# Performance work log

Hardware: AMD Instinct MI355X
Metric: run time of the kernel (lower is better)

## Reference

```python
import jax, jax.numpy as jnp
import numpy as np

N_NODES = 50000
N_EDGES = 800000


def _gcn_layer(x, edges, W, b):
    # support = x @ W  (dense transform first: cheaper when out_dim < in_dim)
    support = x @ W  # [N, D_out]
    src, dst = edges[0], edges[1]
    # sparse neighbor aggregation: sum_{(s,d) in E} support[s] into node d
    agg = jax.ops.segment_sum(support[src], dst, num_segments=x.shape[0])
    return agg + b


def setup_inputs() -> dict:
    key = jax.random.key(0)
    k1, k2, k3, k4, k5, k6 = jax.random.split(key, 6)
    x = jax.random.normal(k1, (N_NODES, 512), dtype=jnp.float32)
    edges = jax.random.randint(k2, (2, N_EDGES), 0, N_NODES, dtype=jnp.int32)
    W1 = jax.random.normal(k3, (512, 256), dtype=jnp.float32) * 0.05
    b1 = jax.random.normal(k4, (256,), dtype=jnp.float32) * 0.05
    W2 = jax.random.normal(k5, (256, 128), dtype=jnp.float32) * 0.05
    b2 = jax.random.normal(k6, (128,), dtype=jnp.float32) * 0.05
    return {"x": x, "edges": edges, "W1": W1, "b1": b1, "W2": W2, "b2": b2}


def reference(x, edges, W1, b1, W2, b2):
    x1 = jax.nn.relu(_gcn_layer(x, edges, W1, b1))
    x2 = jax.nn.relu(_gcn_layer(x1, edges, W2, b2))
    return x2
```

## Files before the change

### kernel.cpp

```cpp
#include <hip/hip_runtime.h>

#define N_NODES 50000
#define N_EDGES 800000
#define MP 50176
#define CAP 64

typedef unsigned short ushort_t;
typedef unsigned int uint_t;
using short8 = __attribute__((ext_vector_type(8))) short;
using f32x4 = __attribute__((ext_vector_type(4))) float;
using floatx2 = __attribute__((ext_vector_type(2))) float;
using int4v = __attribute__((ext_vector_type(4))) int;
using uint4v = __attribute__((ext_vector_type(4))) uint_t;

__device__ __forceinline__ ushort_t f2bf(float f) {
    uint_t u;
    __builtin_memcpy(&u, &f, 4);
    u = u + 0x7FFF + ((u >> 16) & 1);
    return (ushort_t)(u >> 16);
}

__global__ __launch_bounds__(256) void prep(const float* __restrict__ W1,
                                            const float* __restrict__ W2,
                                            ushort_t* __restrict__ W1t,
                                            ushort_t* __restrict__ W2t,
                                            int* __restrict__ cnt) {
    const int i = blockIdx.x * blockDim.x + threadIdx.x;
    if (i < 256 * 512) {
        const int n = i >> 9, k = i & 511;
        W1t[i] = f2bf(W1[(size_t)k * 256 + n]);
    }
    if (i < 128 * 256) {
        const int n = i >> 8, k = i & 255;
        W2t[i] = f2bf(W2[(size_t)k * 128 + n]);
    }
    if (i < N_NODES) cnt[i] = 0;
}

__global__ __launch_bounds__(256) void csr_fill_bucket(
    const int* __restrict__ eg, int* __restrict__ cnt,
    int* __restrict__ csrp) {
    constexpr int PART = N_NODES / 8;
    const int part = blockIdx.x & 7;
    const int q = blockIdx.x >> 3;
    const int lo = part * PART;
    const int hi = lo + PART;
    const int stride = (gridDim.x >> 3) * 256;
    for (int e = q * 256 + threadIdx.x; e < N_EDGES; e += stride) {
        const int d = eg[N_EDGES + e];
        if (d >= lo && d < hi) {
            const int slot = atomicAdd(&cnt[d], 1);
            if (slot < CAP) csrp[(size_t)d * CAP + slot] = eg[e];
        }
    }
}

template <int K, int BN, bool AF32, bool CFP8>
__global__ __launch_bounds__(512) void gemm_mfma(const void* __restrict__ Av,
                                                 const ushort_t* __restrict__ Bt,
                                                 void* __restrict__ Cv) {
    constexpr int KT = K / 64;
    constexpr int NF = BN / 64;
    constexpr int BSL = (BN == 256) ? 4 : 2;
    __shared__ ushort_t lA[128 * 64];
    __shared__ ushort_t lB[BN * 64];
    const int tid = threadIdx.x;
    const int w = tid >> 6, lane = tid & 63;
    const int wr = w >> 2, wc = w & 3;
    const int m0 = blockIdx.x * 128;

    const int ar = tid >> 2, aq0 = (tid & 3) * 2;
    const int br = (BN == 256) ? (tid >> 1) : (tid >> 2);
    const int bs0 = (BN == 256) ? ((tid & 1) * 4) : ((tid & 3) * 2);

    int agr = m0 + ar;
    if (AF32 && agr >= N_NODES) agr = 0;

    f32x4 acc[4][NF];
#pragma unroll
    for (int m = 0; m < 4; ++m)
#pragma unroll
        for (int n = 0; n < NF; ++n) acc[m][n] = (f32x4){0.f, 0.f, 0.f, 0.f};

    float4 fa[4];
    int4v ha0, ha1;
    int4v rB[BSL];

    auto LOAD = [&](int kt) {
        if constexpr (AF32) {
            const float* Af = (const float*)Av;
            const float4* p =
                (const float4*)(Af + (size_t)agr * K + kt * 64 + aq0 * 8);
#pragma unroll
            for (int i = 0; i < 4; ++i) fa[i] = p[i];
        } else {
            const ushort_t* Ab = (const ushort_t*)Av;
            const int4v* p =
                (const int4v*)(Ab + (size_t)(m0 + ar) * K + kt * 64 + aq0 * 8);
            ha0 = p[0];
            ha1 = p[1];
        }
        const int4v* qp = (const int4v*)(Bt + (size_t)br * K + kt * 64 + bs0 * 8);
#pragma unroll
        for (int s = 0; s < BSL; ++s) rB[s] = qp[s];
    };

    auto STORE = [&]() {
        short8 oa0, oa1;
        if constexpr (AF32) {
            oa0[0] = (short)f2bf(fa[0].x); oa0[1] = (short)f2bf(fa[0].y);
            oa0[2] = (short)f2bf(fa[0].z); oa0[3] = (short)f2bf(fa[0].w);
            oa0[4] = (short)f2bf(fa[1].x); oa0[5] = (short)f2bf(fa[1].y);
            oa0[6] = (short)f2bf(fa[1].z); oa0[7] = (short)f2bf(fa[1].w);
            oa1[0] = (short)f2bf(fa[2].x); oa1[1] = (short)f2bf(fa[2].y);
            oa1[2] = (short)f2bf(fa[2].z); oa1[3] = (short)f2bf(fa[2].w);
            oa1[4] = (short)f2bf(fa[3].x); oa1[5] = (short)f2bf(fa[3].y);
            oa1[6] = (short)f2bf(fa[3].z); oa1[7] = (short)f2bf(fa[3].w);
        } else {
            __builtin_memcpy(&oa0, &ha0, 16);
            __builtin_memcpy(&oa1, &ha1, 16);
        }
        *(short8*)((char*)lA + ar * 128 + ((aq0 ^ (ar & 7)) << 4)) = oa0;
        *(short8*)((char*)lA + ar * 128 + (((aq0 + 1) ^ (ar & 7)) << 4)) = oa1;
#pragma unroll
        for (int s = 0; s < BSL; ++s) {
            short8 ob;
            __builtin_memcpy(&ob, &rB[s], 16);
            *(short8*)((char*)lB + br * 128 + (((bs0 + s) ^ (br & 7)) << 4)) = ob;
        }
    };

    LOAD(0);
    STORE();
    __syncthreads();

    for (int kt = 0; kt < KT; ++kt) {
        if (kt + 1 < KT) LOAD(kt + 1);
        __builtin_amdgcn_sched_barrier(0);
        const int g = lane >> 4, rr = lane & 15;
#pragma unroll
        for (int kk = 0; kk < 2; ++kk) {
            short8 av[4], bv[NF];
#pragma unroll
            for (int m = 0; m < 4; ++m) {
                const int row = wr * 64 + m * 16 + rr;
                av[m] = *(const short8*)((const char*)lA + row * 128 +
                                         (((kk * 4 + g) ^ (row & 7)) << 4));
            }
#pragma unroll
            for (int n = 0; n < NF; ++n) {
                const int row = wc * (BN / 4) + n * 16 + rr;
                bv[n] = *(const short8*)((const char*)lB + row * 128 +
                                         (((kk * 4 + g) ^ (row & 7)) << 4));
            }
#pragma unroll
            for (int m = 0; m < 4; ++m)
#pragma unroll
                for (int n = 0; n < NF; ++n)
                    acc[m][n] = __builtin_amdgcn_mfma_f32_16x16x32_bf16(
                        av[m], bv[n], acc[m][n], 0, 0, 0);
        }
        __syncthreads();
        if (kt + 1 < KT) {
            STORE();
            __syncthreads();
        }
    }

    const int rr = lane & 15, rg = lane >> 4;
#pragma unroll
    for (int m = 0; m < 4; ++m)
#pragma unroll
        for (int n = 0; n < NF; ++n) {
            const int row0 = m0 + wr * 64 + m * 16 + rg * 4;
            const int col = wc * (BN / 4) + n * 16 + rr;
            if constexpr (CFP8) {
                unsigned char* Cb = (unsigned char*)Cv;
                const int w01 = __builtin_amdgcn_cvt_pk_fp8_f32(
                    acc[m][n][0], acc[m][n][1], 0, false);
                const int w23 = __builtin_amdgcn_cvt_pk_fp8_f32(
                    acc[m][n][2], acc[m][n][3], 0, false);
                Cb[(size_t)(row0 + 0) * BN + col] = (unsigned char)(w01 & 0xff);
                Cb[(size_t)(row0 + 1) * BN + col] = (unsigned char)((w01 >> 8) & 0xff);
                Cb[(size_t)(row0 + 2) * BN + col] = (unsigned char)(w23 & 0xff);
                Cb[(size_t)(row0 + 3) * BN + col] = (unsigned char)((w23 >> 8) & 0xff);
            } else {
                ushort_t* Cs = (ushort_t*)Cv;
#pragma unroll
                for (int q = 0; q < 4; ++q)
                    Cs[(size_t)(row0 + q) * BN + col] = f2bf(acc[m][n][q]);
            }
        }
}

template <int D, bool MASKED>
__device__ __forceinline__ void chunk8_fp8(const unsigned char* __restrict__ S,
                                           const int* __restrict__ csr,
                                           int j, int end, int coff,
                                           float* __restrict__ acc) {
    int id[8];
#pragma unroll
    for (int q = 0; q < 8; ++q) {
        const int raw = csr[j + q];
        id[q] = (!MASKED || (j + q < end)) ? raw : 0;
    }
    uint4v v[8];
#pragma unroll
    for (int q = 0; q < 8; ++q)
        v[q] = *(const uint4v*)(S + (size_t)id[q] * D + coff);
#pragma unroll
    for (int q = 0; q < 8; ++q) {
        const float mq = MASKED ? ((j + q < end) ? 1.f : 0.f) : 1.f;
#pragma unroll
        for (int wd = 0; wd < 4; ++wd) {
            const int word = (int)v[q][wd];
            const floatx2 lo = __builtin_amdgcn_cvt_pk_f32_fp8(word, false);
            const floatx2 hi = __builtin_amdgcn_cvt_pk_f32_fp8(word, true);
            if (MASKED) {
                acc[wd * 4 + 0] = fmaf(mq, lo[0], acc[wd * 4 + 0]);
                acc[wd * 4 + 1] = fmaf(mq, lo[1], acc[wd * 4 + 1]);
                acc[wd * 4 + 2] = fmaf(mq, hi[0], acc[wd * 4 + 2]);
                acc[wd * 4 + 3] = fmaf(mq, hi[1], acc[wd * 4 + 3]);
            } else {
                acc[wd * 4 + 0] += lo[0];
                acc[wd * 4 + 1] += lo[1];
                acc[wd * 4 + 2] += hi[0];
                acc[wd * 4 + 3] += hi[1];
            }
        }
    }
}

template <int D, bool OUT_BF16>
__global__ __launch_bounds__(256) void gather_fp8(
    const unsigned char* __restrict__ S, const int* __restrict__ cnt,
    const int* __restrict__ csrp, const float* __restrict__ bias,
    void* __restrict__ out) {
    constexpr int LPN = D / 16;
    const int gtid = blockIdx.x * blockDim.x + threadIdx.x;
    const int node = gtid / LPN;
    const int l = gtid % LPN;
    if (node >= N_NODES) return;
    const int beg = node * CAP;
    const int deg = min(cnt[node], CAP);
    const int end = beg + deg;
    const int coff = l * 16;

    float acc[16];
#pragma unroll
    for (int k = 0; k < 16; ++k) acc[k] = 0.f;

    int j = beg;
    const int e8 = beg + (deg & ~7);
    for (; j < e8; j += 8) chunk8_fp8<D, false>(S, csrp, j, end, coff, acc);
    if (j < end) chunk8_fp8<D, true>(S, csrp, j, end, coff, acc);

#pragma unroll
    for (int k = 0; k < 16; ++k) acc[k] = fmaxf(acc[k] + bias[coff + k], 0.f);

    if (OUT_BF16) {
        short8 o0, o1;
#pragma unroll
        for (int k = 0; k < 8; ++k) {
            o0[k] = (short)f2bf(acc[k]);
            o1[k] = (short)f2bf(acc[8 + k]);
        }
        ushort_t* op = (ushort_t*)out + (size_t)node * D + coff;
        *(short8*)(op) = o0;
        *(short8*)(op + 8) = o1;
    } else {
        float* op = (float*)out + (size_t)node * D + coff;
        *(float4*)(op + 0)  = make_float4(acc[0], acc[1], acc[2], acc[3]);
        *(float4*)(op + 4)  = make_float4(acc[4], acc[5], acc[6], acc[7]);
        *(float4*)(op + 8)  = make_float4(acc[8], acc[9], acc[10], acc[11]);
        *(float4*)(op + 12) = make_float4(acc[12], acc[13], acc[14], acc[15]);
    }
}

extern "C" void kernel_launch(void* const* d_in, const int* in_sizes, int n_in,
                              void* d_out, int out_size, void* d_ws, size_t ws_size,
                              hipStream_t stream) {
    const float* x  = (const float*)d_in[0];
    const int*   eg = (const int*)d_in[1];
    const float* W1 = (const float*)d_in[2];
    const float* b1 = (const float*)d_in[3];
    const float* W2 = (const float*)d_in[4];
    const float* b2 = (const float*)d_in[5];
    float* out = (float*)d_out;

    char* ws = (char*)d_ws;
    const size_t SUP1_OFF = 0;
    const size_t AGG1_OFF = 25690112;
    const size_t SUP2_OFF = 51380224;
    const size_t W1T_OFF  = 77070336;
    const size_t W2T_OFF  = 77332480;
    const size_t CNT_OFF  = 77398016;
    const size_t CSRP_OFF = 77598208;

    unsigned char* sup1 = (unsigned char*)(ws + SUP1_OFF);
    ushort_t* agg1 = (ushort_t*)(ws + AGG1_OFF);
    unsigned char* sup2 = (unsigned char*)(ws + SUP2_OFF);
    ushort_t* W1t  = (ushort_t*)(ws + W1T_OFF);
    ushort_t* W2t  = (ushort_t*)(ws + W2T_OFF);
    int* cnt  = (int*)(ws + CNT_OFF);
    int* csrp = (int*)(ws + CSRP_OFF);

    prep<<<512, 256, 0, stream>>>(W1, W2, W1t, W2t, cnt);
    csr_fill_bucket<<<2048, 256, 0, stream>>>(eg, cnt, csrp);

    gemm_mfma<512, 256, true, true><<<MP / 128, 512, 0, stream>>>(x, W1t, sup1);
    gather_fp8<256, true><<<(N_NODES * 16 + 255) / 256, 256, 0, stream>>>(
        sup1, cnt, csrp, b1, agg1);

    gemm_mfma<256, 128, false, true><<<MP / 128, 512, 0, stream>>>(agg1, W2t, sup2);
    gather_fp8<128, false><<<(N_NODES * 8 + 255) / 256, 256, 0, stream>>>(
        sup2, cnt, csrp, b2, out);
}
```

Measured before the change: 142.4 us.

## Use direct global-to-LDS async loads with double-buffered tiles in both GEMMs

Splits the templated GEMM into two specialized kernels. B tiles (and A tiles in the second GEMM) are loaded straight into LDS with global_load_lds into double buffers, with pre-swizzled source addresses, so the register staging and LDS store pass go away and the next tile's load overlaps the current compute. The cost is more LDS per block (64KB+ for gemm1), which may lower occupancy. Correctness also depends on the async LDS writes being complete at the barriers, since no explicit vmcnt wait is added.

```diff
diff --git a/kernel.cpp b/kernel.cpp
--- a/kernel.cpp
+++ b/kernel.cpp
@@ -18,6 +18,12 @@
     __builtin_memcpy(&u, &f, 4);
     u = u + 0x7FFF + ((u >> 16) & 1);
     return (ushort_t)(u >> 16);
+}
+
+__device__ __forceinline__ void async_copy16(const void* g, void* l) {
+    __builtin_amdgcn_global_load_lds(
+        (const __attribute__((address_space(1))) uint_t*)g,
+        (__attribute__((address_space(3))) uint_t*)l, 16, 0, 0);
 }
 
 __global__ __launch_bounds__(256) void prep(const float* __restrict__ W1,
@@ -55,92 +61,75 @@
     }
 }
 
-template <int K, int BN, bool AF32, bool CFP8>
-__global__ __launch_bounds__(512) void gemm_mfma(const void* __restrict__ Av,
-                                                 const ushort_t* __restrict__ Bt,
-                                                 void* __restrict__ Cv) {
-    constexpr int KT = K / 64;
-    constexpr int NF = BN / 64;
-    constexpr int BSL = (BN == 256) ? 4 : 2;
+__global__ __launch_bounds__(512) void gemm1_k(const float* __restrict__ A,
+                                               const ushort_t* __restrict__ Bt,
+                                               unsigned char* __restrict__ C) {
+    constexpr int K = 512, BN = 256, KT = 8;
     __shared__ ushort_t lA[128 * 64];
-    __shared__ ushort_t lB[BN * 64];
+    __shared__ ushort_t lB[2][256 * 64];
     const int tid = threadIdx.x;
     const int w = tid >> 6, lane = tid & 63;
     const int wr = w >> 2, wc = w & 3;
     const int m0 = blockIdx.x * 128;
 
     const int ar = tid >> 2, aq0 = (tid & 3) * 2;
-    const int br = (BN == 256) ? (tid >> 1) : (tid >> 2);
-    const int bs0 = (BN == 256) ? ((tid & 1) * 4) : ((tid & 3) * 2);
+    const int sr = lane >> 3, sj = lane & 7;
 
     int agr = m0 + ar;
-    if (AF32 && agr >= N_NODES) agr = 0;
-
-    f32x4 acc[4][NF];
+    if (agr >= N_NODES) agr = 0;
+
+    f32x4 acc[4][4];
 #pragma unroll
     for (int m = 0; m < 4; ++m)
 #pragma unroll
-        for (int n = 0; n < NF; ++n) acc[m][n] = (f32x4){0.f, 0.f, 0.f, 0.f};
+        for (int n = 0; n < 4; ++n) acc[m][n] = (f32x4){0.f, 0.f, 0.f, 0.f};
 
     float4 fa[4];
-    int4v ha0, ha1;
-    int4v rB[BSL];
-
-    auto LOAD = [&](int kt) {
-        if constexpr (AF32) {
-            const float* Af = (const float*)Av;
-            const float4* p =
-                (const float4*)(Af + (size_t)agr * K + kt * 64 + aq0 * 8);
-#pragma unroll
-            for (int i = 0; i < 4; ++i) fa[i] = p[i];
-        } else {
-            const ushort_t* Ab = (const ushort_t*)Av;
-            const int4v* p =
-                (const int4v*)(Ab + (size_t)(m0 + ar) * K + kt * 64 + aq0 * 8);
-            ha0 = p[0];
-            ha1 = p[1];
-        }
-        const int4v* qp = (const int4v*)(Bt + (size_t)br * K + kt * 64 + bs0 * 8);
-#pragma unroll
-        for (int s = 0; s < BSL; ++s) rB[s] = qp[s];
+
+    auto LOAD_A = [&](int kt) {
+        const float4* p = (const float4*)(A + (size_t)agr * K + kt * 64 + aq0 * 8);
+#pragma unroll
+        for (int i = 0; i < 4; ++i) fa[i] = p[i];
     };
-
-    auto STORE = [&]() {
+    auto ISSUE_B = [&](int kt, int buf) {
+#pragma unroll
+        for (int i = 0; i < 4; ++i) {
+            const int r = w * 32 + i * 8 + sr;
+            const char* g = (const char*)Bt + ((size_t)r * K + kt * 64) * 2 +
+                            ((size_t)(sj ^ (r & 7)) << 4);
+            async_copy16(g, lB[buf] + (size_t)(w * 32 + i * 8) * 64);
+        }
+    };
+    auto STORE_A = [&]() {
         short8 oa0, oa1;
-        if constexpr (AF32) {
-            oa0[0] = (short)f2bf(fa[0].x); oa0[1] = (short)f2bf(fa[0].y);
-            oa0[2] = (short)f2bf(fa[0].z); oa0[3] = (short)f2bf(fa[0].w);
-            oa0[4] = (short)f2bf(fa[1].x); oa0[5] = (short)f2bf(fa[1].y);
-            oa0[6] = (short)f2bf(fa[1].z); oa0[7] = (short)f2bf(fa[1].w);
-            oa1[0] = (short)f2bf(fa[2].x); oa1[1] = (short)f2bf(fa[2].y);
-            oa1[2] = (short)f2bf(fa[2].z); oa1[3] = (short)f2bf(fa[2].w);
-            oa1[4] = (short)f2bf(fa[3].x); oa1[5] = (short)f2bf(fa[3].y);
-            oa1[6] = (short)f2bf(fa[3].z); oa1[7] = (short)f2bf(fa[3].w);
-        } else {
-            __builtin_memcpy(&oa0, &ha0, 16);
-            __builtin_memcpy(&oa1, &ha1, 16);
-        }
+        oa0[0] = (short)f2bf(fa[0].x); oa0[1] = (short)f2bf(fa[0].y);
+        oa0[2] = (short)f2bf(fa[0].z); oa0[3] = (short)f2bf(fa[0].w);
+        oa0[4] = (short)f2bf(fa[1].x); oa0[5] = (short)f2bf(fa[1].y);
+        oa0[6] = (short)f2bf(fa[1].z); oa0[7] = (short)f2bf(fa[1].w);
+        oa1[0] = (short)f2bf(fa[2].x); oa1[1] = (short)f2bf(fa[2].y);
+        oa1[2] = (short)f2bf(fa[2].z); oa1[3] = (short)f2bf(fa[2].w);
+        oa1[4] = (short)f2bf(fa[3].x); oa1[5] = (short)f2bf(fa[3].y);
+        oa1[6] = (short)f2bf(fa[3].z); oa1[7] = (short)f2bf(fa[3].w);
         *(short8*)((char*)lA + ar * 128 + ((aq0 ^ (ar & 7)) << 4)) = oa0;
         *(short8*)((char*)lA + ar * 128 + (((aq0 + 1) ^ (ar & 7)) << 4)) = oa1;
-#pragma unroll
-        for (int s = 0; s < BSL; ++s) {
-            short8 ob;
-            __builtin_memcpy(&ob, &rB[s], 16);
-            *(short8*)((char*)lB + br * 128 + (((bs0 + s) ^ (br & 7)) << 4)) = ob;
-        }
     };
 
-    LOAD(0);
-    STORE();
+    LOAD_A(0);
+    ISSUE_B(0, 0);
+    STORE_A();
     __syncthreads();
 
+    int cur = 0;
     for (int kt = 0; kt < KT; ++kt) {
-        if (kt + 1 < KT) LOAD(kt + 1);
+        if (kt + 1 < KT) {
+            ISSUE_B(kt + 1, cur ^ 1);
+            LOAD_A(kt + 1);
+        }
         __builtin_amdgcn_sched_barrier(0);
         const int g = lane >> 4, rr = lane & 15;
 #pragma unroll
         for (int kk = 0; kk < 2; ++kk) {
-            short8 av[4], bv[NF];
+            short8 av[4], bv[4];
 #pragma unroll
             for (int m = 0; m < 4; ++m) {
                 const int row = wr * 64 + m * 16 + rr;
@@ -148,21 +137,22 @@
                                          (((kk * 4 + g) ^ (row & 7)) << 4));
             }
 #pragma unroll
-            for (int n = 0; n < NF; ++n) {
-                const int row = wc * (BN / 4) + n * 16 + rr;
-                bv[n] = *(const short8*)((const char*)lB + row * 128 +
+            for (int n = 0; n < 4; ++n) {
+                const int row = wc * 64 + n * 16 + rr;
+                bv[n] = *(const short8*)((const char*)lB[cur] + row * 128 +
                                          (((kk * 4 + g) ^ (row & 7)) << 4));
             }
 #pragma unroll
             for (int m = 0; m < 4; ++m)
 #pragma unroll
-                for (int n = 0; n < NF; ++n)
+                for (int n = 0; n < 4; ++n)
                     acc[m][n] = __builtin_amdgcn_mfma_f32_16x16x32_bf16(
                         av[m], bv[n], acc[m][n], 0, 0, 0);
         }
         __syncthreads();
         if (kt + 1 < KT) {
-            STORE();
+            STORE_A();
+            cur ^= 1;
             __syncthreads();
         }
     }
@@ -171,25 +161,100 @@
 #pragma unroll
     for (int m = 0; m < 4; ++m)
 #pragma unroll
-        for (int n = 0; n < NF; ++n) {
+        for (int n = 0; n < 4; ++n) {
             const int row0 = m0 + wr * 64 + m * 16 + rg * 4;
-            const int col = wc * (BN / 4) + n * 16 + rr;
-            if constexpr (CFP8) {
-                unsigned char* Cb = (unsigned char*)Cv;
-                const int w01 = __builtin_amdgcn_cvt_pk_fp8_f32(
-                    acc[m][n][0], acc[m][n][1], 0, false);
-                const int w23 = __builtin_amdgcn_cvt_pk_fp8_f32(
-                    acc[m][n][2], acc[m][n][3], 0, false);
-                Cb[(size_t)(row0 + 0) * BN + col] = (unsigned char)(w01 & 0xff);
-                Cb[(size_t)(row0 + 1) * BN + col] = (unsigned char)((w01 >> 8) & 0xff);
-                Cb[(size_t)(row0 + 2) * BN + col] = (unsigned char)(w23 & 0xff);
-                Cb[(size_t)(row0 + 3) * BN + col] = (unsigned char)((w23 >> 8) & 0xff);
-            } else {
-                ushort_t* Cs = (ushort_t*)Cv;
-#pragma unroll
-                for (int q = 0; q < 4; ++q)
-                    Cs[(size_t)(row0 + q) * BN + col] = f2bf(acc[m][n][q]);
-            }
+            const int col = wc * 64 + n * 16 + rr;
+            const int w01 = __builtin_amdgcn_cvt_pk_fp8_f32(
+                acc[m][n][0], acc[m][n][1], 0, false);
+            const int w23 = __builtin_amdgcn_cvt_pk_fp8_f32(
+                acc[m][n][2], acc[m][n][3], 0, false);
+            C[(size_t)(row0 + 0) * BN + col] = (unsigned char)(w01 & 0xff);
+            C[(size_t)(row0 + 1) * BN + col] = (unsigned char)((w01 >> 8) & 0xff);
+            C[(size_t)(row0 + 2) * BN + col] = (unsigned char)(w23 & 0xff);
+            C[(size_t)(row0 + 3) * BN + col] = (unsigned char)((w23 >> 8) & 0xff);
+        }
+}
+
+__global__ __launch_bounds__(512) void gemm2_k(const ushort_t* __restrict__ A,
+                                               const ushort_t* __restrict__ Bt,
+                                               unsigned char* __restrict__ C) {
+    constexpr int K = 256, BN = 128, KT = 4;
+    __shared__ ushort_t lA[2][128 * 64];
+    __shared__ ushort_t lB[2][128 * 64];
+    const int tid = threadIdx.x;
+    const int w = tid >> 6, lane = tid & 63;
+    const int wr = w >> 2, wc = w & 3;
+    const int m0 = blockIdx.x * 128;
+    const int sr = lane >> 3, sj = lane & 7;
+
+    f32x4 acc[4][2];
+#pragma unroll
+    for (int m = 0; m < 4; ++m)
+#pragma unroll
+        for (int n = 0; n < 2; ++n) acc[m][n] = (f32x4){0.f, 0.f, 0.f, 0.f};
+
+    auto ISSUE = [&](int kt, int buf) {
+#pragma unroll
+        for (int i = 0; i < 2; ++i) {
+            const int r = w * 16 + i * 8 + sr;
+            const char* ga = (const char*)A + ((size_t)(m0 + r) * K + kt * 64) * 2 +
+                             ((size_t)(sj ^ (r & 7)) << 4);
+            async_copy16(ga, lA[buf] + (size_t)(w * 16 + i * 8) * 64);
+            const char* gb = (const char*)Bt + ((size_t)r * K + kt * 64) * 2 +
+                             ((size_t)(sj ^ (r & 7)) << 4);
+            async_copy16(gb, lB[buf] + (size_t)(w * 16 + i * 8) * 64);
+        }
+    };
+
+    ISSUE(0, 0);
+    __syncthreads();
+
+    int cur = 0;
+    for (int kt = 0; kt < KT; ++kt) {
+        if (kt + 1 < KT) ISSUE(kt + 1, cur ^ 1);
+        __builtin_amdgcn_sched_barrier(0);
+        const int g = lane >> 4, rr = lane & 15;
+#pragma unroll
+        for (int kk = 0; kk < 2; ++kk) {
+            short8 av[4], bv[2];
+#pragma unroll
+            for (int m = 0; m < 4; ++m) {
+                const int row = wr * 64 + m * 16 + rr;
+                av[m] = *(const short8*)((const char*)lA[cur] + row * 128 +
+                                         (((kk * 4 + g) ^ (row & 7)) << 4));
+            }
+#pragma unroll
+            for (int n = 0; n < 2; ++n) {
+                const int row = wc * 32 + n * 16 + rr;
+                bv[n] = *(const short8*)((const char*)lB[cur] + row * 128 +
+                                         (((kk * 4 + g) ^ (row & 7)) << 4));
+            }
+#pragma unroll
+            for (int m = 0; m < 4; ++m)
+#pragma unroll
+                for (int n = 0; n < 2; ++n)
+                    acc[m][n] = __builtin_amdgcn_mfma_f32_16x16x32_bf16(
+                        av[m], bv[n], acc[m][n], 0, 0, 0);
+        }
+        __syncthreads();
+        cur ^= 1;
+    }
+
+    const int rr = lane & 15, rg = lane >> 4;
+#pragma unroll
+    for (int m = 0; m < 4; ++m)
+#pragma unroll
+        for (int n = 0; n < 2; ++n) {
+            const int row0 = m0 + wr * 64 + m * 16 + rg * 4;
+            const int col = wc * 32 + n * 16 + rr;
+            const int w01 = __builtin_amdgcn_cvt_pk_fp8_f32(
+                acc[m][n][0], acc[m][n][1], 0, false);
+            const int w23 = __builtin_amdgcn_cvt_pk_fp8_f32(
+                acc[m][n][2], acc[m][n][3], 0, false);
+            C[(size_t)(row0 + 0) * BN + col] = (unsigned char)(w01 & 0xff);
+            C[(size_t)(row0 + 1) * BN + col] = (unsigned char)((w01 >> 8) & 0xff);
+            C[(size_t)(row0 + 2) * BN + col] = (unsigned char)(w23 & 0xff);
+            C[(size_t)(row0 + 3) * BN + col] = (unsigned char)((w23 >> 8) & 0xff);
         }
 }
 
@@ -308,11 +373,11 @@
     prep<<<512, 256, 0, stream>>>(W1, W2, W1t, W2t, cnt);
     csr_fill_bucket<<<2048, 256, 0, stream>>>(eg, cnt, csrp);
 
-    gemm_mfma<512, 256, true, true><<<MP / 128, 512, 0, stream>>>(x, W1t, sup1);
+    gemm1_k<<<MP / 128, 512, 0, stream>>>(x, W1t, sup1);
     gather_fp8<256, true><<<(N_NODES * 16 + 255) / 256, 256, 0, stream>>>(
         sup1, cnt, csrp, b1, agg1);
 
-    gemm_mfma<256, 128, false, true><<<MP / 128, 512, 0, stream>>>(agg1, W2t, sup2);
+    gemm2_k<<<MP / 128, 512, 0, stream>>>(agg1, W2t, sup2);
     gather_fp8<128, false><<<(N_NODES * 8 + 255) / 256, 256, 0, stream>>>(
         sup2, cnt, csrp, b2, out);
 }
```

Result: slower. 145.2 us (+2.0%).
